# Kernel optimization log

Measured on AMD Instinct MI355X. Metric: run time of the kernel, lower is better.

The kernel has to match this reference:

```python
import jax, jax.numpy as jnp
import numpy as np

NUM_EMBEDDINGS = 4096
EMBEDDING_DIM = 128
COMMITMENT_COST = 0.25


def setup_inputs() -> dict:
    key = jax.random.key(0)
    k_x, k_w = jax.random.split(key)
    inputs = jax.random.normal(k_x, (32, 128, 32, 32), dtype=jnp.float32)
    # xavier_uniform for Embedding weight [K, D]: bound = sqrt(6/(K+D))
    bound = float(np.sqrt(6.0 / (NUM_EMBEDDINGS + EMBEDDING_DIM)))
    weight = jax.random.uniform(k_w, (NUM_EMBEDDINGS, EMBEDDING_DIM),
                                dtype=jnp.float32, minval=-bound, maxval=bound)
    return {"inputs": inputs, "weight": weight}


def reference(inputs, weight):
    K, D = weight.shape
    # channels-first 4D input with C == embedding_dim -> NHWC
    x = jnp.transpose(inputs, (0, 2, 3, 1))  # [B, H, W, D]
    input_shape = x.shape
    flat = x.reshape(-1, D)                  # [N, D]

    x_sq = jnp.sum(flat * flat, axis=1, keepdims=True)          # [N, 1]
    w_sq = jnp.sum(weight * weight, axis=1)                     # [K]
    two_xy = 2.0 * jnp.matmul(flat, weight.T)                   # [N, K]
    distances = x_sq - two_xy + w_sq[None, :] + 1e-8

    encoding_indices = jnp.argmin(distances, axis=1)            # [N] int

    quantized = weight[encoding_indices].reshape(input_shape)   # [B, H, W, D]

    q_latent_loss = jnp.mean((quantized - x) ** 2)
    e_latent_loss = jnp.mean((jax.lax.stop_gradient(quantized) - x) ** 2)
    loss = q_latent_loss + COMMITMENT_COST * e_latent_loss
    loss = jnp.where(jnp.isnan(loss) | jnp.isinf(loss), jnp.float32(0.1), loss)

    quantized_st = x + jax.lax.stop_gradient(quantized - x)

    counts = jnp.zeros((K,), dtype=jnp.float32).at[encoding_indices].add(1.0)
    avg_probs = counts / encoding_indices.shape[0]
    perplexity = jnp.exp(-jnp.sum(avg_probs * jnp.log(avg_probs + 1e-10)))

    encodings = jax.nn.one_hot(encoding_indices, K, dtype=jnp.float32)  # [N, K]

    # input was channels-first -> restore NCHW
    quantized_st = jnp.transpose(quantized_st, (0, 3, 1, 2))
    return quantized_st, loss, perplexity, encodings, encoding_indices
```

## Files before the change

### kernel.cpp

```cpp
#include <hip/hip_runtime.h>
#include <stdint.h>
#include <math.h>

#define K_CODES 4096
#define DIM 128
#define N_FLAT 32768
#define HW 1024

#define OFF_Q    0
#define OFF_LOSS 4194304
#define OFF_PERP 4194305
#define OFF_ENC  4194306
#define OFF_IDX  138412034

#define WS_PACKED 0
#define WS_COUNTS 262144
#define WS_WSQ    278528
#define WS_XSQ    294912
#define WS_PART   425984
#define WS_XHL    430080
#define WS_WHL    (WS_XHL + 16777216)

typedef _Float16 f16x8 __attribute__((ext_vector_type(8)));
typedef float    f32x4 __attribute__((ext_vector_type(4)));


__global__ __launch_bounds__(64) void wsq_kernel(const float* __restrict__ w,
                                                 float* __restrict__ wsq) {
    int k = blockIdx.x;
    int lane = threadIdx.x;
    float a = w[k * DIM + lane];
    float b = w[k * DIM + lane + 64];
    float s = a * a + b * b;
    #pragma unroll
    for (int o = 32; o > 0; o >>= 1) s += __shfl_down(s, o, 64);
    if (lane == 0) wsq[k] = s;
}

__global__ __launch_bounds__(256) void xsq_kernel(const float* __restrict__ x,
                                                  float* __restrict__ xsq) {
    int n = blockIdx.x * 256 + threadIdx.x;
    int b = n >> 10, hw = n & 1023;
    const float* xb = x + (size_t)b * (DIM * HW) + hw;
    float s = 0.f;
    #pragma unroll
    for (int c = 0; c < DIM; ++c) {
        float v = xb[c * HW];
        s = fmaf(v, v, s);
    }
    xsq[n] = s;
}

__global__ __launch_bounds__(256) void xplanes_kernel(const float* __restrict__ x,
                                                      _Float16* __restrict__ xhl) {
    __shared__ float xt[128 * 65];
    const int t = threadIdx.x;
    const int n0 = blockIdx.x * 64;
    const int b = n0 >> 10, hw0 = n0 & 1023;
    const float* xg = x + (size_t)b * (DIM * HW) + hw0;
    #pragma unroll
    for (int i = 0; i < 16; ++i) {
        int idx = i * 256 + t;
        int c = idx >> 5, n2 = (idx & 31) << 1;
        float2 v = *(const float2*)(xg + c * HW + n2);
        xt[c * 65 + n2] = v.x;
        xt[c * 65 + n2 + 1] = v.y;
    }
    __syncthreads();
    const int n = t >> 2, seg = t & 3;
    _Float16* row = xhl + (size_t)(n0 + n) * 256;
    #pragma unroll
    for (int q = 0; q < 4; ++q) {
        f16x8 hv, lv;
        #pragma unroll
        for (int j = 0; j < 8; ++j) {
            float v = 32.0f * xt[(seg * 32 + q * 8 + j) * 65 + n];
            _Float16 h = (_Float16)v;
            _Float16 l = (_Float16)(v - (float)h);
            hv[j] = h; lv[j] = l;
        }
        *(f16x8*)(row + seg * 32 + q * 8) = hv;
        *(f16x8*)(row + 128 + seg * 32 + q * 8) = lv;
    }
}

__global__ __launch_bounds__(256) void wplanes_kernel(const float* __restrict__ w,
                                                      _Float16* __restrict__ whl) {
    int T = blockIdx.x * 256 + threadIdx.x;
    int k = T >> 2, seg = T & 3;
    const float* wp = w + (size_t)k * DIM + seg * 32;
    _Float16* row = whl + (size_t)k * 256;
    #pragma unroll
    for (int q = 0; q < 4; ++q) {
        float4 a = *(const float4*)(wp + q * 8);
        float4 b = *(const float4*)(wp + q * 8 + 4);
        float vv[8] = {a.x, a.y, a.z, a.w, b.x, b.y, b.z, b.w};
        f16x8 hv, lv;
        #pragma unroll
        for (int j = 0; j < 8; ++j) {
            float v = 1024.0f * vv[j];
            _Float16 h = (_Float16)v;
            _Float16 l = (_Float16)(v - (float)h);
            hv[j] = h; lv[j] = l;
        }
        *(f16x8*)(row + seg * 32 + q * 8) = hv;
        *(f16x8*)(row + 128 + seg * 32 + q * 8) = lv;
    }
}

__global__ __launch_bounds__(256) void dist_argmin(
    const _Float16* __restrict__ xhl, const _Float16* __restrict__ whl,
    const float* __restrict__ wsq, const float* __restrict__ xsq,
    unsigned long long* __restrict__ packed, float* __restrict__ enc)
{
    __shared__ __align__(16) _Float16 xl[128 * 72];
    __shared__ __align__(16) _Float16 wl[128 * 72];
    __shared__ float xsq_s[128], wsq_s[128];
    __shared__ unsigned long long red[128][2];

    const int tid  = threadIdx.x;
    const int lane = tid & 63, wave = tid >> 6;
    const int lq   = lane & 15, quad = lane >> 4;
    const int wn0  = (wave >> 1) * 64, wk0 = (wave & 1) * 64;
    const int n0   = blockIdx.x * 128, k0 = blockIdx.y * 128;

    const int sr = tid >> 3, sh = (tid >> 2) & 1, sq = tid & 3;

    if (tid < 128) { xsq_s[tid] = xsq[n0 + tid]; wsq_s[tid] = wsq[k0 + tid]; }

    {
        float2 z2; z2.x = 0.f; z2.y = 0.f;
        float* ebase = enc + (size_t)n0 * K_CODES + k0;
        #pragma unroll 4
        for (int i = 0; i < 32; ++i) {
            int idx = i * 256 + tid;
            int r = idx >> 6, c2 = idx & 63;
            *(float2*)(ebase + (size_t)r * K_CODES + c2 * 2) = z2;
        }
    }

    f32x4 acc[4][4];
    #pragma unroll
    for (int i = 0; i < 4; ++i)
        #pragma unroll
        for (int j = 0; j < 4; ++j)
            acc[i][j] = (f32x4){0.f, 0.f, 0.f, 0.f};

    const _Float16* xbase = xhl + (size_t)n0 * 256;
    const _Float16* wbase = whl + (size_t)k0 * 256;

    #pragma unroll
    for (int c0 = 0; c0 < 4; ++c0) {
        if (c0 > 0) __syncthreads();
        #pragma unroll
        for (int i = 0; i < 4; ++i) {
            int r = sr + i * 32;
            int goff = r * 256 + sh * 128 + c0 * 32 + sq * 8;
            int loff = r * 72 + sh * 32 + sq * 8;
            *(f16x8*)(xl + loff) = *(const f16x8*)(xbase + goff);
            *(f16x8*)(wl + loff) = *(const f16x8*)(wbase + goff);
        }
        __syncthreads();

        f16x8 ah[4], al[4], bh[4], bl[4];
        #pragma unroll
        for (int i = 0; i < 4; ++i) {
            int xrow = (wn0 + i * 16 + lq) * 72 + quad * 8;
            ah[i] = *(const f16x8*)(xl + xrow);
            al[i] = *(const f16x8*)(xl + xrow + 32);
            int wrow = (wk0 + i * 16 + lq) * 72 + quad * 8;
            bh[i] = *(const f16x8*)(wl + wrow);
            bl[i] = *(const f16x8*)(wl + wrow + 32);
        }
        #pragma unroll
        for (int ki = 0; ki < 4; ++ki)
            #pragma unroll
            for (int ni = 0; ni < 4; ++ni) {
                acc[ni][ki] = __builtin_amdgcn_mfma_f32_16x16x32_f16(
                    ah[ni], bh[ki], acc[ni][ki], 0, 0, 0);
                acc[ni][ki] = __builtin_amdgcn_mfma_f32_16x16x32_f16(
                    ah[ni], bl[ki], acc[ni][ki], 0, 0, 0);
                acc[ni][ki] = __builtin_amdgcn_mfma_f32_16x16x32_f16(
                    al[ni], bh[ki], acc[ni][ki], 0, 0, 0);
            }
    }

    #pragma unroll
    for (int ni = 0; ni < 4; ++ni) {
        #pragma unroll
        for (int rg = 0; rg < 4; ++rg) {
            int rowl = wn0 + ni * 16 + quad * 4 + rg;
            float xr = xsq_s[rowl];
            float best = 3.4e38f; int bk = 0;
            #pragma unroll
            for (int ki = 0; ki < 4; ++ki) {
                int kl = wk0 + ki * 16 + lq;
                float t = xr - acc[ni][ki][rg] * 6.103515625e-05f;
                t += wsq_s[kl];
                t += 1e-8f;
                if (t < best) { best = t; bk = k0 + kl; }
            }
            unsigned u = __float_as_uint(best);
            u = (u & 0x80000000u) ? ~u : (u | 0x80000000u);
            unsigned long long p = ((unsigned long long)u << 32) | (unsigned)bk;
            #pragma unroll
            for (int m = 1; m < 16; m <<= 1) {
                unsigned long long o = __shfl_xor(p, m, 64);
                if (o < p) p = o;
            }
            if (lq == 0) red[rowl][wave & 1] = p;
        }
    }
    __syncthreads();
    if (tid < 128) {
        unsigned long long a = red[tid][0], b = red[tid][1];
        atomicMin(&packed[n0 + tid], a < b ? a : b);
    }
}

__global__ __launch_bounds__(256) void combine(
    const unsigned long long* __restrict__ packed,
    float* __restrict__ idxf, float* __restrict__ enc,
    float* __restrict__ counts)
{
    int n = blockIdx.x * 256 + threadIdx.x;
    unsigned k = (unsigned)(packed[n] & 0xFFFFFFFFu);
    idxf[n] = (float)k;
    enc[(size_t)n * K_CODES + k] = 1.0f;
    atomicAdd(&counts[k], 1.0f);
}

__global__ __launch_bounds__(256) void quantize_loss(
    const float* __restrict__ x, const float* __restrict__ w,
    const float* __restrict__ idxf, float* __restrict__ outq,
    float* __restrict__ part)
{
    const int base4 = (blockIdx.x * 256 + threadIdx.x) * 4;
    float s = 0.f;
    #pragma unroll
    for (int i = 0; i < 4; ++i) {
        int e  = base4 + i * 1048576;
        int hw = e & 1023;
        int c  = (e >> 10) & 127;
        int b  = e >> 17;
        int n  = (b << 10) | hw;
        float4 xv = *(const float4*)(x + e);
        float4 kf = *(const float4*)(idxf + n);
        float q0 = w[(int)kf.x * DIM + c];
        float q1 = w[(int)kf.y * DIM + c];
        float q2 = w[(int)kf.z * DIM + c];
        float q3 = w[(int)kf.w * DIM + c];
        float4 df; df.x = q0 - xv.x; df.y = q1 - xv.y;
                   df.z = q2 - xv.z; df.w = q3 - xv.w;
        float4 o;  o.x = xv.x + df.x; o.y = xv.y + df.y;
                   o.z = xv.z + df.z; o.w = xv.w + df.w;
        *(float4*)(outq + e) = o;
        s = fmaf(df.x, df.x, s);
        s = fmaf(df.y, df.y, s);
        s = fmaf(df.z, df.z, s);
        s = fmaf(df.w, df.w, s);
    }
    #pragma unroll
    for (int o = 32; o > 0; o >>= 1) s += __shfl_down(s, o, 64);
    __shared__ float ls[4];
    if ((threadIdx.x & 63) == 0) ls[threadIdx.x >> 6] = s;
    __syncthreads();
    if (threadIdx.x == 0) part[blockIdx.x] = ls[0] + ls[1] + ls[2] + ls[3];
}

__global__ __launch_bounds__(256) void finalize(
    const float* __restrict__ counts, const float* __restrict__ part,
    float* __restrict__ out)
{
    __shared__ float sh[512];
    float h = 0.f;
    for (int k = threadIdx.x; k < K_CODES; k += 256) {
        float p = counts[k] * (1.0f / N_FLAT);
        h += p * logf(p + 1e-10f);
    }
    float s = 0.f;
    for (int i = threadIdx.x; i < 1024; i += 256) s += part[i];
    sh[threadIdx.x] = h;
    sh[256 + threadIdx.x] = s;
    __syncthreads();
    #pragma unroll
    for (int st = 128; st > 0; st >>= 1) {
        if (threadIdx.x < st) {
            sh[threadIdx.x] += sh[threadIdx.x + st];
            sh[256 + threadIdx.x] += sh[256 + threadIdx.x + st];
        }
        __syncthreads();
    }
    if (threadIdx.x == 0) {
        float perp = expf(-sh[0]);
        float loss = 1.25f * (sh[256] / 4194304.0f);
        if (isnan(loss) || isinf(loss)) loss = 0.1f;
        out[OFF_LOSS] = loss;
        out[OFF_PERP] = perp;
    }
}

extern "C" void kernel_launch(void* const* d_in, const int* in_sizes, int n_in,
                              void* d_out, int out_size, void* d_ws, size_t ws_size,
                              hipStream_t stream) {
    const float* x = (const float*)d_in[0];
    const float* w = (const float*)d_in[1];
    float* out = (float*)d_out;
    char* ws = (char*)d_ws;

    unsigned long long* packed = (unsigned long long*)(ws + WS_PACKED);
    float* counts = (float*)(ws + WS_COUNTS);
    float* wsq    = (float*)(ws + WS_WSQ);
    float* xsq    = (float*)(ws + WS_XSQ);
    float* part   = (float*)(ws + WS_PART);
    _Float16* xhl = (_Float16*)(ws + WS_XHL);
    _Float16* whl = (_Float16*)(ws + WS_WHL);

    hipMemsetAsync(packed, 0xFF, (size_t)N_FLAT * 8, stream);
    hipMemsetAsync(counts, 0, (size_t)K_CODES * 4, stream);

    wsq_kernel<<<K_CODES, 64, 0, stream>>>(w, wsq);
    xsq_kernel<<<N_FLAT / 256, 256, 0, stream>>>(x, xsq);
    xplanes_kernel<<<N_FLAT / 64, 256, 0, stream>>>(x, xhl);
    wplanes_kernel<<<K_CODES * 4 / 256, 256, 0, stream>>>(w, whl);

    dim3 g2(256, 32);
    dist_argmin<<<g2, 256, 0, stream>>>(xhl, whl, wsq, xsq, packed,
                                        out + OFF_ENC);

    combine<<<N_FLAT / 256, 256, 0, stream>>>(packed, out + OFF_IDX,
                                              out + OFF_ENC, counts);

    quantize_loss<<<1024, 256, 0, stream>>>(x, w, out + OFF_IDX,
                                            out + OFF_Q, part);

    finalize<<<1, 256, 0, stream>>>(counts, part, out);
}
```

Baseline: 880.0 us.

## Fuse prep kernels and loop four code tiles per distance block

After: 846.7 us, median of 2. -3.8%, faster.

```diff
diff --git a/kernel.cpp b/kernel.cpp
--- a/kernel.cpp
+++ b/kernel.cpp
@@ -25,34 +25,47 @@
 typedef float    f32x4 __attribute__((ext_vector_type(4)));
 
 
-__global__ __launch_bounds__(64) void wsq_kernel(const float* __restrict__ w,
-                                                 float* __restrict__ wsq) {
-    int k = blockIdx.x;
-    int lane = threadIdx.x;
+__global__ __launch_bounds__(256) void wsq_kernel(const float* __restrict__ w,
+                                                  float* __restrict__ wsq,
+                                                  float* __restrict__ counts) {
+    int wave = threadIdx.x >> 6, lane = threadIdx.x & 63;
+    int k = blockIdx.x * 4 + wave;
     float a = w[k * DIM + lane];
     float b = w[k * DIM + lane + 64];
     float s = a * a + b * b;
     #pragma unroll
     for (int o = 32; o > 0; o >>= 1) s += __shfl_down(s, o, 64);
-    if (lane == 0) wsq[k] = s;
-}
-
-__global__ __launch_bounds__(256) void xsq_kernel(const float* __restrict__ x,
-                                                  float* __restrict__ xsq) {
-    int n = blockIdx.x * 256 + threadIdx.x;
-    int b = n >> 10, hw = n & 1023;
-    const float* xb = x + (size_t)b * (DIM * HW) + hw;
-    float s = 0.f;
-    #pragma unroll
-    for (int c = 0; c < DIM; ++c) {
-        float v = xb[c * HW];
-        s = fmaf(v, v, s);
-    }
-    xsq[n] = s;
-}
-
-__global__ __launch_bounds__(256) void xplanes_kernel(const float* __restrict__ x,
-                                                      _Float16* __restrict__ xhl) {
+    if (lane == 0) { wsq[k] = s; counts[k] = 0.f; }
+}
+
+__global__ __launch_bounds__(256) void wplanes_kernel(const float* __restrict__ w,
+                                                      _Float16* __restrict__ whl) {
+    int T = blockIdx.x * 256 + threadIdx.x;
+    int k = T >> 2, seg = T & 3;
+    const float* wp = w + (size_t)k * DIM + seg * 32;
+    _Float16* row = whl + (size_t)k * 256;
+    #pragma unroll
+    for (int q = 0; q < 4; ++q) {
+        float4 a = *(const float4*)(wp + q * 8);
+        float4 b = *(const float4*)(wp + q * 8 + 4);
+        float vv[8] = {a.x, a.y, a.z, a.w, b.x, b.y, b.z, b.w};
+        f16x8 hv, lv;
+        #pragma unroll
+        for (int j = 0; j < 8; ++j) {
+            float v = 1024.0f * vv[j];
+            _Float16 h = (_Float16)v;
+            _Float16 l = (_Float16)(v - (float)h);
+            hv[j] = h; lv[j] = l;
+        }
+        *(f16x8*)(row + seg * 32 + q * 8) = hv;
+        *(f16x8*)(row + 128 + seg * 32 + q * 8) = lv;
+    }
+}
+
+__global__ __launch_bounds__(256) void xprep_kernel(const float* __restrict__ x,
+                                                    _Float16* __restrict__ xhl,
+                                                    float* __restrict__ xsq,
+                                                    unsigned long long* __restrict__ packed) {
     __shared__ float xt[128 * 65];
     const int t = threadIdx.x;
     const int n0 = blockIdx.x * 64;
@@ -67,6 +80,16 @@
         xt[c * 65 + n2 + 1] = v.y;
     }
     __syncthreads();
+    if (t < 64) {
+        packed[n0 + t] = ~0ull;
+        float s = 0.f;
+        #pragma unroll
+        for (int c = 0; c < DIM; ++c) {
+            float v = xt[c * 65 + t];
+            s = fmaf(v, v, s);
+        }
+        xsq[n0 + t] = s;
+    }
     const int n = t >> 2, seg = t & 3;
     _Float16* row = xhl + (size_t)(n0 + n) * 256;
     #pragma unroll
@@ -75,30 +98,6 @@
         #pragma unroll
         for (int j = 0; j < 8; ++j) {
             float v = 32.0f * xt[(seg * 32 + q * 8 + j) * 65 + n];
-            _Float16 h = (_Float16)v;
-            _Float16 l = (_Float16)(v - (float)h);
-            hv[j] = h; lv[j] = l;
-        }
-        *(f16x8*)(row + seg * 32 + q * 8) = hv;
-        *(f16x8*)(row + 128 + seg * 32 + q * 8) = lv;
-    }
-}
-
-__global__ __launch_bounds__(256) void wplanes_kernel(const float* __restrict__ w,
-                                                      _Float16* __restrict__ whl) {
-    int T = blockIdx.x * 256 + threadIdx.x;
-    int k = T >> 2, seg = T & 3;
-    const float* wp = w + (size_t)k * DIM + seg * 32;
-    _Float16* row = whl + (size_t)k * 256;
-    #pragma unroll
-    for (int q = 0; q < 4; ++q) {
-        float4 a = *(const float4*)(wp + q * 8);
-        float4 b = *(const float4*)(wp + q * 8 + 4);
-        float vv[8] = {a.x, a.y, a.z, a.w, b.x, b.y, b.z, b.w};
-        f16x8 hv, lv;
-        #pragma unroll
-        for (int j = 0; j < 8; ++j) {
-            float v = 1024.0f * vv[j];
             _Float16 h = (_Float16)v;
             _Float16 l = (_Float16)(v - (float)h);
             hv[j] = h; lv[j] = l;
@@ -122,99 +121,110 @@
     const int lane = tid & 63, wave = tid >> 6;
     const int lq   = lane & 15, quad = lane >> 4;
     const int wn0  = (wave >> 1) * 64, wk0 = (wave & 1) * 64;
-    const int n0   = blockIdx.x * 128, k0 = blockIdx.y * 128;
+    const int n0   = blockIdx.x * 128;
+    const int kbase = blockIdx.y * 512;
 
     const int sr = tid >> 3, sh = (tid >> 2) & 1, sq = tid & 3;
 
-    if (tid < 128) { xsq_s[tid] = xsq[n0 + tid]; wsq_s[tid] = wsq[k0 + tid]; }
-
     {
-        float2 z2; z2.x = 0.f; z2.y = 0.f;
-        float* ebase = enc + (size_t)n0 * K_CODES + k0;
-        #pragma unroll 4
-        for (int i = 0; i < 32; ++i) {
+        float* ebase = enc + (size_t)n0 * K_CODES + kbase;
+        float4 z4; z4.x = z4.y = z4.z = z4.w = 0.f;
+        #pragma unroll 8
+        for (int i = 0; i < 64; ++i) {
             int idx = i * 256 + tid;
-            int r = idx >> 6, c2 = idx & 63;
-            *(float2*)(ebase + (size_t)r * K_CODES + c2 * 2) = z2;
-        }
-    }
-
-    f32x4 acc[4][4];
-    #pragma unroll
-    for (int i = 0; i < 4; ++i)
-        #pragma unroll
-        for (int j = 0; j < 4; ++j)
-            acc[i][j] = (f32x4){0.f, 0.f, 0.f, 0.f};
+            int r = idx >> 7, c4 = idx & 127;
+            *(float4*)(ebase + (size_t)r * K_CODES + 2 + c4 * 4) = z4;
+        }
+        if (tid < 128) {
+            float2 z2; z2.x = 0.f; z2.y = 0.f;
+            *(float2*)(ebase + (size_t)tid * K_CODES) = z2;
+        }
+    }
+
+    if (tid < 128) xsq_s[tid] = xsq[n0 + tid];
 
     const _Float16* xbase = xhl + (size_t)n0 * 256;
-    const _Float16* wbase = whl + (size_t)k0 * 256;
-
-    #pragma unroll
-    for (int c0 = 0; c0 < 4; ++c0) {
-        if (c0 > 0) __syncthreads();
-        #pragma unroll
-        for (int i = 0; i < 4; ++i) {
-            int r = sr + i * 32;
-            int goff = r * 256 + sh * 128 + c0 * 32 + sq * 8;
-            int loff = r * 72 + sh * 32 + sq * 8;
-            *(f16x8*)(xl + loff) = *(const f16x8*)(xbase + goff);
-            *(f16x8*)(wl + loff) = *(const f16x8*)(wbase + goff);
+
+    for (int ks = 0; ks < 4; ++ks) {
+        const int k0 = kbase + ks * 128;
+        if (tid < 128) wsq_s[tid] = wsq[k0 + tid];
+        const _Float16* wbase = whl + (size_t)k0 * 256;
+
+        f32x4 acc[4][4];
+        #pragma unroll
+        for (int i = 0; i < 4; ++i)
+            #pragma unroll
+            for (int j = 0; j < 4; ++j)
+                acc[i][j] = (f32x4){0.f, 0.f, 0.f, 0.f};
+
+        #pragma unroll
+        for (int c0 = 0; c0 < 4; ++c0) {
+            __syncthreads();
+            #pragma unroll
+            for (int i = 0; i < 4; ++i) {
+                int r = sr + i * 32;
+                int goff = r * 256 + sh * 128 + c0 * 32 + sq * 8;
+                int loff = r * 72 + sh * 32 + sq * 8;
+                *(f16x8*)(xl + loff) = *(const f16x8*)(xbase + goff);
+                *(f16x8*)(wl + loff) = *(const f16x8*)(wbase + goff);
+            }
+            __syncthreads();
+
+            f16x8 ah[4], al[4], bh[4], bl[4];
+            #pragma unroll
+            for (int i = 0; i < 4; ++i) {
+                int xrow = (wn0 + i * 16 + lq) * 72 + quad * 8;
+                ah[i] = *(const f16x8*)(xl + xrow);
+                al[i] = *(const f16x8*)(xl + xrow + 32);
+                int wrow = (wk0 + i * 16 + lq) * 72 + quad * 8;
+                bh[i] = *(const f16x8*)(wl + wrow);
+                bl[i] = *(const f16x8*)(wl + wrow + 32);
+            }
+            #pragma unroll
+            for (int ki = 0; ki < 4; ++ki)
+                #pragma unroll
+                for (int ni = 0; ni < 4; ++ni) {
+                    acc[ni][ki] = __builtin_amdgcn_mfma_f32_16x16x32_f16(
+                        ah[ni], bh[ki], acc[ni][ki], 0, 0, 0);
+                    acc[ni][ki] = __builtin_amdgcn_mfma_f32_16x16x32_f16(
+                        ah[ni], bl[ki], acc[ni][ki], 0, 0, 0);
+                    acc[ni][ki] = __builtin_amdgcn_mfma_f32_16x16x32_f16(
+                        al[ni], bh[ki], acc[ni][ki], 0, 0, 0);
+                }
+        }
+
+        #pragma unroll
+        for (int ni = 0; ni < 4; ++ni) {
+            #pragma unroll
+            for (int rg = 0; rg < 4; ++rg) {
+                int rowl = wn0 + ni * 16 + quad * 4 + rg;
+                float xr = xsq_s[rowl];
+                float best = 3.4e38f; int bk = 0;
+                #pragma unroll
+                for (int ki = 0; ki < 4; ++ki) {
+                    int kl = wk0 + ki * 16 + lq;
+                    float t = xr - acc[ni][ki][rg] * 6.103515625e-05f;
+                    t += wsq_s[kl];
+                    t += 1e-8f;
+                    if (t < best) { best = t; bk = k0 + kl; }
+                }
+                unsigned u = __float_as_uint(best);
+                u = (u & 0x80000000u) ? ~u : (u | 0x80000000u);
+                unsigned long long p =
+                    ((unsigned long long)u << 32) | (unsigned)bk;
+                #pragma unroll
+                for (int m = 1; m < 16; m <<= 1) {
+                    unsigned long long o = __shfl_xor(p, m, 64);
+                    if (o < p) p = o;
+                }
+                if (lq == 0) red[rowl][wave & 1] = p;
+            }
         }
         __syncthreads();
-
-        f16x8 ah[4], al[4], bh[4], bl[4];
-        #pragma unroll
-        for (int i = 0; i < 4; ++i) {
-            int xrow = (wn0 + i * 16 + lq) * 72 + quad * 8;
-            ah[i] = *(const f16x8*)(xl + xrow);
-            al[i] = *(const f16x8*)(xl + xrow + 32);
-            int wrow = (wk0 + i * 16 + lq) * 72 + quad * 8;
-            bh[i] = *(const f16x8*)(wl + wrow);
-            bl[i] = *(const f16x8*)(wl + wrow + 32);
-        }
-        #pragma unroll
-        for (int ki = 0; ki < 4; ++ki)
-            #pragma unroll
-            for (int ni = 0; ni < 4; ++ni) {
-                acc[ni][ki] = __builtin_amdgcn_mfma_f32_16x16x32_f16(
-                    ah[ni], bh[ki], acc[ni][ki], 0, 0, 0);
-                acc[ni][ki] = __builtin_amdgcn_mfma_f32_16x16x32_f16(
-                    ah[ni], bl[ki], acc[ni][ki], 0, 0, 0);
-                acc[ni][ki] = __builtin_amdgcn_mfma_f32_16x16x32_f16(
-                    al[ni], bh[ki], acc[ni][ki], 0, 0, 0);
-            }
-    }
-
-    #pragma unroll
-    for (int ni = 0; ni < 4; ++ni) {
-        #pragma unroll
-        for (int rg = 0; rg < 4; ++rg) {
-            int rowl = wn0 + ni * 16 + quad * 4 + rg;
-            float xr = xsq_s[rowl];
-            float best = 3.4e38f; int bk = 0;
-            #pragma unroll
-            for (int ki = 0; ki < 4; ++ki) {
-                int kl = wk0 + ki * 16 + lq;
-                float t = xr - acc[ni][ki][rg] * 6.103515625e-05f;
-                t += wsq_s[kl];
-                t += 1e-8f;
-                if (t < best) { best = t; bk = k0 + kl; }
-            }
-            unsigned u = __float_as_uint(best);
-            u = (u & 0x80000000u) ? ~u : (u | 0x80000000u);
-            unsigned long long p = ((unsigned long long)u << 32) | (unsigned)bk;
-            #pragma unroll
-            for (int m = 1; m < 16; m <<= 1) {
-                unsigned long long o = __shfl_xor(p, m, 64);
-                if (o < p) p = o;
-            }
-            if (lq == 0) red[rowl][wave & 1] = p;
-        }
-    }
-    __syncthreads();
-    if (tid < 128) {
-        unsigned long long a = red[tid][0], b = red[tid][1];
-        atomicMin(&packed[n0 + tid], a < b ? a : b);
+        if (tid < 128) {
+            unsigned long long a = red[tid][0], b = red[tid][1];
+            atomicMin(&packed[n0 + tid], a < b ? a : b);
+        }
     }
 }
 
@@ -316,15 +326,11 @@
     _Float16* xhl = (_Float16*)(ws + WS_XHL);
     _Float16* whl = (_Float16*)(ws + WS_WHL);
 
-    hipMemsetAsync(packed, 0xFF, (size_t)N_FLAT * 8, stream);
-    hipMemsetAsync(counts, 0, (size_t)K_CODES * 4, stream);
-
-    wsq_kernel<<<K_CODES, 64, 0, stream>>>(w, wsq);
-    xsq_kernel<<<N_FLAT / 256, 256, 0, stream>>>(x, xsq);
-    xplanes_kernel<<<N_FLAT / 64, 256, 0, stream>>>(x, xhl);
+    wsq_kernel<<<K_CODES / 4, 256, 0, stream>>>(w, wsq, counts);
     wplanes_kernel<<<K_CODES * 4 / 256, 256, 0, stream>>>(w, whl);
-
-    dim3 g2(256, 32);
+    xprep_kernel<<<N_FLAT / 64, 256, 0, stream>>>(x, xhl, xsq, packed);
+
+    dim3 g2(256, 8);
     dist_argmin<<<g2, 256, 0, stream>>>(xhl, whl, wsq, xsq, packed,
                                         out + OFF_ENC);
 
```
